# Performance work log

Measured on AMD Instinct MI355X. Metric: run time of the kernel, lower is better.

## Reference

```python
import jax, jax.numpy as jnp
import numpy as np

B, H, W, C = 16, 56, 56, 512
NUM_HEADS = 8
WS = 4  # window_size


def setup_inputs() -> dict:
    key = jax.random.key(0)
    k1, k2, k3, k4 = jax.random.split(key, 4)
    x = jax.random.normal(k1, (B, H, W, C), dtype=jnp.float32)
    w_qkv_h = jax.random.normal(k2, (3 * C, C), dtype=jnp.float32) * 0.02
    w_qkv_l = jax.random.normal(k3, (3 * C, C), dtype=jnp.float32) * 0.02
    w_proj = jax.random.normal(k4, (C, 2 * C), dtype=jnp.float32) * 0.02
    b_proj = jnp.zeros((C,), dtype=jnp.float32)
    return {"x": x, "w_qkv_h": w_qkv_h, "w_qkv_l": w_qkv_l,
            "w_proj": w_proj, "b_proj": b_proj}


def reference(x, w_qkv_h, w_qkv_l, w_proj, b_proj):
    b, h, w, c = x.shape
    nh = NUM_HEADS
    hd = c // nh
    nw = WS * WS  # tokens per window
    scale = c ** -0.5  # NOTE: original scales by full dim, not head dim

    # window partition: [B*H/ws*W/ws, ws*ws, C]
    xw = x.reshape(b, h // WS, WS, w // WS, WS, c)
    xw = xw.transpose(0, 1, 3, 2, 4, 5).reshape(-1, nw, c)

    # local branch qkv: [3, Nwin, nh, nw, hd]
    qkv_h = (xw @ w_qkv_h.T).reshape(-1, nw, 3, nh, hd).transpose(2, 0, 3, 1, 4)
    q_h, k_h, v_h = qkv_h[0], qkv_h[1], qkv_h[2]

    # global branch: average-pool each window to a single token [Nwin, 1, C]
    x_avg = x.reshape(b, h // WS, WS, w // WS, WS, c).mean(axis=(2, 4))
    x_avg = x_avg.reshape(-1, 1, c)
    qkv_l = (x_avg @ w_qkv_l.T).reshape(-1, 1, 3, nh, hd).transpose(2, 0, 3, 1, 4)
    q_l, k_l, v_l = qkv_l[0], qkv_l[1], qkv_l[2]

    # local window attention: [Nwin, nh, nw, nw]
    attn_h = jax.nn.softmax(jnp.einsum('bhqd,bhkd->bhqk', q_h, k_h) * scale, axis=-1)
    x_h = jnp.einsum('bhqk,bhkd->bhqd', attn_h, v_h)
    x_h = x_h.transpose(0, 2, 1, 3).reshape(-1, nw, c)

    # pooled global attention (1 token -> softmax over singleton = 1)
    attn_l = jax.nn.softmax(jnp.einsum('bhqd,bhkd->bhqk', q_l, k_l) * scale, axis=-1)
    x_l = jnp.einsum('bhqk,bhkd->bhqd', attn_l, v_l)
    x_l = x_l.transpose(0, 2, 1, 3).reshape(-1, 1, c)

    # concat local + broadcast global, project 2C -> C
    x_out = jnp.concatenate([x_h, jnp.broadcast_to(x_l, (x_l.shape[0], nw, c))], axis=-1)
    x_out = x_out @ w_proj.T + b_proj

    # window reverse
    x_out = x_out.reshape(b, h // WS, w // WS, WS, WS, c)
    x_out = x_out.transpose(0, 1, 3, 2, 4, 5).reshape(b, h, w, c)
    return x_out
```

## Files before the change

### kernel.cpp

```cpp
#include <hip/hip_runtime.h>


using bf16x8 = __attribute__((ext_vector_type(8))) short;
using f32x4  = __attribute__((ext_vector_type(4))) float;

#define SCALE 0.044194173824159216f

__device__ __forceinline__ unsigned short f2bf(float f) {
    union { float f; unsigned u; } v; v.f = f;
    unsigned u = v.u;
    return (unsigned short)((u + 0x7fffu + ((u >> 16) & 1u)) >> 16);
}

__device__ __forceinline__ void gl2lds16(const unsigned short* g, unsigned short* l) {
    __builtin_amdgcn_global_load_lds(
        (const __attribute__((address_space(1))) void*)g,
        (__attribute__((address_space(3))) void*)l, 16, 0, 0);
}

__global__ void k_prep_weights(const float* __restrict__ wqkv_h,
                               const float* __restrict__ wqkv_l,
                               const float* __restrict__ wproj,
                               unsigned short* __restrict__ WH,
                               unsigned short* __restrict__ WLV,
                               unsigned short* __restrict__ WP1,
                               unsigned short* __restrict__ WP2) {
    int i = blockIdx.x * 256 + threadIdx.x;
    if (i < 786432) {
        WH[i] = f2bf(wqkv_h[i]);
    } else {
        int j = i - 786432;
        int r = j >> 18;
        int t = j & 262143;
        int n = t >> 9, k = t & 511;
        if (r == 0)      WLV[t] = f2bf(wqkv_l[(1024 + n) * 512 + k]);
        else if (r == 1) WP1[t] = f2bf(wproj[n * 1024 + k]);
        else             WP2[t] = f2bf(wproj[n * 1024 + 512 + k]);
    }
}

__global__ void k_window_pool(const float* __restrict__ x,
                              unsigned short* __restrict__ XW,
                              unsigned short* __restrict__ XAVG) {
    int win = blockIdx.x * 2 + (threadIdx.x >> 7);
    int g = threadIdx.x & 127;
    int c = g * 4;
    int b = win / 196, rem = win % 196, wh = rem / 14, ww = rem % 14;
    float4 s = {0.f, 0.f, 0.f, 0.f};
    #pragma unroll
    for (int t = 0; t < 16; ++t) {
        int row = (b * 56 + wh * 4 + (t >> 2)) * 56 + ww * 4 + (t & 3);
        float4 v = *(const float4*)&x[(size_t)row * 512 + c];
        uint2 pk;
        pk.x = (unsigned)f2bf(v.x) | ((unsigned)f2bf(v.y) << 16);
        pk.y = (unsigned)f2bf(v.z) | ((unsigned)f2bf(v.w) << 16);
        *(uint2*)&XW[(size_t)(win * 16 + t) * 512 + c] = pk;
        s.x += v.x; s.y += v.y; s.z += v.z; s.w += v.w;
    }
    uint2 pa;
    pa.x = (unsigned)f2bf(s.x * 0.0625f) | ((unsigned)f2bf(s.y * 0.0625f) << 16);
    pa.y = (unsigned)f2bf(s.z * 0.0625f) | ((unsigned)f2bf(s.w * 0.0625f) << 16);
    *(uint2*)&XAVG[(size_t)win * 512 + c] = pa;
}

template <int NT>
__global__ void k_gemm512(const unsigned short* __restrict__ A,
                          const unsigned short* __restrict__ Bw,
                          unsigned short* __restrict__ outB,
                          float* __restrict__ outF,
                          const float* __restrict__ bias) {
    int wave = threadIdx.x >> 6, lane = threadIdx.x & 63;
    int quad = lane >> 4, l16 = lane & 15;
    int m0 = blockIdx.x * 64 + wave * 16;
    int n0 = blockIdx.y * (NT * 16);
    f32x4 acc[NT] = {};
    const unsigned short* arow = A + (size_t)(m0 + l16) * 512 + quad * 8;
    for (int kk = 0; kk < 16; ++kk) {
        bf16x8 a = *(const bf16x8*)(arow + kk * 32);
        #pragma unroll
        for (int nt = 0; nt < NT; ++nt) {
            bf16x8 b = *(const bf16x8*)(Bw + (size_t)(n0 + nt * 16 + l16) * 512 + kk * 32 + quad * 8);
            acc[nt] = __builtin_amdgcn_mfma_f32_16x16x32_bf16(a, b, acc[nt], 0, 0, 0);
        }
    }
    #pragma unroll
    for (int nt = 0; nt < NT; ++nt) {
        int col = n0 + nt * 16 + l16;
        float bv = (bias != nullptr) ? bias[col] : 0.f;
        #pragma unroll
        for (int r = 0; r < 4; ++r) {
            int row = m0 + quad * 4 + r;
            if (outF != nullptr) outF[(size_t)row * 512 + col] = acc[nt][r] + bv;
            else                 outB[(size_t)row * 512 + col] = f2bf(acc[nt][r]);
        }
    }
}

__global__ void __launch_bounds__(512, 4) k_fused(const unsigned short* __restrict__ XW,
                                                  const unsigned short* __restrict__ WH,
                                                  unsigned short* __restrict__ XH) {
    __shared__ __align__(16) char smem[81920];

    const int tid  = threadIdx.x;
    const int wave = tid >> 6, lane = tid & 63;
    const int quad = lane >> 4, l16 = lane & 15;
    const int mh = wave >> 2, nq = wave & 3;

    int id   = blockIdx.y * 392 + blockIdx.x;
    int s_   = id >> 3;
    int tb   = (id & 7) * 49 + (s_ >> 3);
    int head = s_ & 7;
    const int m0 = tb * 128;

    size_t aof[2];
    #pragma unroll
    for (int i = 0; i < 2; ++i) {
        int u = i * 512 + tid;
        int n = u >> 3;
        int gu = (u & 7) ^ (n & 7);
        aof[i] = (size_t)(m0 + n) * 512 + gu * 8;
    }
    size_t bof[3];
    #pragma unroll
    for (int i = 0; i < 3; ++i) {
        int u = i * 512 + tid;
        int n = u >> 3;
        int gu = (u & 7) ^ (n & 7);
        int nrow = (n >> 6) * 512 + head * 64 + (n & 63);
        bof[i] = (size_t)nrow * 512 + gu * 8;
    }

    unsigned short* const bufA[2] = { (unsigned short*)smem,
                                      (unsigned short*)(smem + 40960) };
    unsigned short* const bufB[2] = { (unsigned short*)(smem + 16384),
                                      (unsigned short*)(smem + 40960 + 16384) };

    f32x4 acc[4][3] = {};
    const int sx = l16 & 7;

    #pragma unroll
    for (int i = 0; i < 2; ++i)
        gl2lds16(XW + aof[i], bufA[0] + (i * 512 + wave * 64) * 8);
    #pragma unroll
    for (int i = 0; i < 3; ++i)
        gl2lds16(WH + bof[i], bufB[0] + (i * 512 + wave * 64) * 8);
    __syncthreads();

    #pragma unroll
    for (int ch = 0; ch < 8; ++ch) {
        unsigned short* As = bufA[ch & 1];
        unsigned short* Bs = bufB[ch & 1];
        if (ch < 7) {
            unsigned short* An = bufA[(ch + 1) & 1];
            unsigned short* Bn = bufB[(ch + 1) & 1];
            #pragma unroll
            for (int i = 0; i < 2; ++i)
                gl2lds16(XW + aof[i] + (ch + 1) * 64, An + (i * 512 + wave * 64) * 8);
            #pragma unroll
            for (int i = 0; i < 3; ++i)
                gl2lds16(WH + bof[i] + (ch + 1) * 64, Bn + (i * 512 + wave * 64) * 8);
        }
        #pragma unroll
        for (int kk = 0; kk < 2; ++kk) {
            int su = ((kk * 4 + quad) ^ sx) * 8;
            bf16x8 a[4], b[3];
            #pragma unroll
            for (int mf = 0; mf < 4; ++mf) {
                int row = mh * 64 + mf * 16 + l16;
                a[mf] = *(const bf16x8*)&As[row * 64 + (((kk * 4 + quad) ^ (row & 7)) ^ sx ^ (row & 7)) * 8];
            }
            #pragma unroll
            for (int j = 0; j < 3; ++j) {
                int brow = nq * 48 + j * 16 + l16;
                b[j] = *(const bf16x8*)&Bs[brow * 64 + (((kk * 4 + quad) ^ (brow & 7)) ^ sx ^ (brow & 7)) * 8];
            }
            #pragma unroll
            for (int mf = 0; mf < 4; ++mf)
                #pragma unroll
                for (int j = 0; j < 3; ++j)
                    acc[mf][j] = __builtin_amdgcn_mfma_f32_16x16x32_bf16(a[mf], b[j], acc[mf][j], 0, 0, 0);
        }
        __syncthreads();
    }

    {
        char* att = smem + mh * 33792;
        unsigned short* qs  = (unsigned short*)att;
        unsigned short* ks  = (unsigned short*)(att + 9216);
        unsigned short* vts = (unsigned short*)(att + 18432);
        #pragma unroll
        for (int j = 0; j < 3; ++j) {
            int cb = nq * 48 + j * 16;
            #pragma unroll
            for (int mf = 0; mf < 4; ++mf) {
                #pragma unroll
                for (int r = 0; r < 4; ++r) {
                    int tok = mf * 16 + quad * 4 + r;
                    unsigned short hv = f2bf(acc[mf][j][r]);
                    if (cb < 64)       qs[tok * 72 + cb + l16] = hv;
                    else if (cb < 128) ks[tok * 72 + (cb - 64) + l16] = hv;
                    else               vts[(cb - 128 + l16) * 88 + tok] = hv;
                }
            }
        }
    }
    __syncthreads();

    char* att = smem + (wave >> 2) * 33792;
    unsigned short* qs  = (unsigned short*)att;
    unsigned short* ks  = (unsigned short*)(att + 9216);
    unsigned short* vts = (unsigned short*)(att + 18432);
    unsigned short* Ps  = (unsigned short*)(att + 29696);
    const int lw = wave & 3, t0 = lw * 16;

    if (lw == 3) {
        #pragma unroll
        for (int i = 0; i < 16; ++i) vts[lane * 88 + 64 + i] = 0;
    }
    {
        int prow = lane >> 2, pc = 16 + (lane & 3) * 4;
        #pragma unroll
        for (int i = 0; i < 4; ++i) Ps[lw * 512 + prow * 32 + pc + i] = 0;
    }

    f32x4 sacc = {};
    {
        bf16x8 a0 = *(const bf16x8*)&qs[(t0 + l16) * 72 + quad * 8];
        bf16x8 b0 = *(const bf16x8*)&ks[(t0 + l16) * 72 + quad * 8];
        sacc = __builtin_amdgcn_mfma_f32_16x16x32_bf16(a0, b0, sacc, 0, 0, 0);
        bf16x8 a1 = *(const bf16x8*)&qs[(t0 + l16) * 72 + 32 + quad * 8];
        bf16x8 b1 = *(const bf16x8*)&ks[(t0 + l16) * 72 + 32 + quad * 8];
        sacc = __builtin_amdgcn_mfma_f32_16x16x32_bf16(a1, b1, sacc, 0, 0, 0);
    }
    float p[4];
    #pragma unroll
    for (int r = 0; r < 4; ++r) {
        float v = sacc[r] * SCALE;
        float m = v;
        m = fmaxf(m, __shfl_xor(m, 1));
        m = fmaxf(m, __shfl_xor(m, 2));
        m = fmaxf(m, __shfl_xor(m, 4));
        m = fmaxf(m, __shfl_xor(m, 8));
        float e = __expf(v - m);
        float sm = e;
        sm += __shfl_xor(sm, 1);
        sm += __shfl_xor(sm, 2);
        sm += __shfl_xor(sm, 4);
        sm += __shfl_xor(sm, 8);
        p[r] = e / sm;
    }
    #pragma unroll
    for (int r = 0; r < 4; ++r)
        Ps[lw * 512 + (quad * 4 + r) * 32 + l16] = f2bf(p[r]);

    bf16x8 pa = *(const bf16x8*)&Ps[lw * 512 + l16 * 32 + quad * 8];
    #pragma unroll
    for (int nt = 0; nt < 4; ++nt) {
        f32x4 y = {};
        bf16x8 bv = *(const bf16x8*)&vts[(nt * 16 + l16) * 88 + t0 + quad * 8];
        y = __builtin_amdgcn_mfma_f32_16x16x32_bf16(pa, bv, y, 0, 0, 0);
        #pragma unroll
        for (int r = 0; r < 4; ++r)
            XH[(size_t)(m0 + (wave >> 2) * 64 + t0 + quad * 4 + r) * 512 + head * 64 + nt * 16 + l16] = f2bf(y[r]);
    }
}

__global__ void __launch_bounds__(256, 2) k_gemm_proj(const unsigned short* __restrict__ XH,
                                                      const unsigned short* __restrict__ WP1,
                                                      const float* __restrict__ G,
                                                      float* __restrict__ out) {
    __shared__ __align__(16) char smem[65536];

    const int wave = threadIdx.x >> 6, lane = threadIdx.x & 63;
    const int quad = lane >> 4, l16 = lane & 15;

    int id = blockIdx.y * 392 + blockIdx.x;
    int s  = id >> 3;
    int xb = (id & 7) * 49 + (s >> 2);
    int yb = s & 3;
    const int m0 = xb * 128, n0 = yb * 128;
    const int wm = (wave >> 1) * 64;
    const int wn = (wave & 1) * 64;

    size_t aofs[4], bofs[4];
    #pragma unroll
    for (int i = 0; i < 4; ++i) {
        int u = (wave * 4 + i) * 64 + lane;
        int n = u >> 3;
        int gu = (lane & 7) ^ (n & 7);
        aofs[i] = (size_t)(m0 + n) * 512 + gu * 8;
        bofs[i] = (size_t)(n0 + n) * 512 + gu * 8;
    }

    unsigned short* const bufA[2] = { (unsigned short*)smem,
                                      (unsigned short*)(smem + 32768) };
    unsigned short* const bufB[2] = { (unsigned short*)(smem + 16384),
                                      (unsigned short*)(smem + 32768 + 16384) };

    f32x4 acc[4][4] = {};
    const int sx = l16 & 7;

    #pragma unroll
    for (int i = 0; i < 4; ++i) {
        gl2lds16(XH + aofs[i], bufA[0] + (wave * 4 + i) * 512);
        gl2lds16(WP1 + bofs[i], bufB[0] + (wave * 4 + i) * 512);
    }
    __syncthreads();

    #pragma unroll
    for (int ch = 0; ch < 8; ++ch) {
        unsigned short* As = bufA[ch & 1];
        unsigned short* Bs = bufB[ch & 1];
        if (ch < 7) {
            unsigned short* An = bufA[(ch + 1) & 1];
            unsigned short* Bn = bufB[(ch + 1) & 1];
            #pragma unroll
            for (int i = 0; i < 4; ++i) {
                gl2lds16(XH + aofs[i] + (ch + 1) * 64, An + (wave * 4 + i) * 512);
                gl2lds16(WP1 + bofs[i] + (ch + 1) * 64, Bn + (wave * 4 + i) * 512);
            }
        }
        #pragma unroll
        for (int kk = 0; kk < 2; ++kk) {
            int su = ((kk * 4 + quad) ^ sx) * 8;
            bf16x8 a[4], b[4];
            #pragma unroll
            for (int mf = 0; mf < 4; ++mf)
                a[mf] = *(const bf16x8*)&As[(wm + mf * 16 + l16) * 64 + su];
            #pragma unroll
            for (int j = 0; j < 4; ++j)
                b[j] = *(const bf16x8*)&Bs[(wn + j * 16 + l16) * 64 + su];
            #pragma unroll
            for (int mf = 0; mf < 4; ++mf)
                #pragma unroll
                for (int j = 0; j < 4; ++j)
                    acc[mf][j] = __builtin_amdgcn_mfma_f32_16x16x32_bf16(a[mf], b[j], acc[mf][j], 0, 0, 0);
        }
        __syncthreads();
    }

    #pragma unroll
    for (int mf = 0; mf < 4; ++mf) {
        #pragma unroll
        for (int r = 0; r < 4; ++r) {
            int tl  = wm + mf * 16 + quad * 4 + r;
            int gt  = m0 + tl;
            int win = gt >> 4, tw = gt & 15;
            int bb = win / 196, rem = win % 196;
            int wh = rem / 14, ww = rem % 14;
            int orow = (bb * 56 + wh * 4 + (tw >> 2)) * 56 + ww * 4 + (tw & 3);
            #pragma unroll
            for (int j = 0; j < 4; ++j) {
                int ncol = n0 + wn + j * 16 + l16;
                out[(size_t)orow * 512 + ncol] = acc[mf][j][r] + G[(size_t)win * 512 + ncol];
            }
        }
    }
}

extern "C" void kernel_launch(void* const* d_in, const int* in_sizes, int n_in,
                              void* d_out, int out_size, void* d_ws, size_t ws_size,
                              hipStream_t stream) {
    const float* x      = (const float*)d_in[0];
    const float* wqkv_h = (const float*)d_in[1];
    const float* wqkv_l = (const float*)d_in[2];
    const float* wproj  = (const float*)d_in[3];
    const float* bproj  = (const float*)d_in[4];
    float* out = (float*)d_out;

    char* ws = (char*)d_ws;
    unsigned short* WH   = (unsigned short*)(ws + 0);
    unsigned short* WLV  = (unsigned short*)(ws + 1572864);
    unsigned short* WP1  = (unsigned short*)(ws + 2097152);
    unsigned short* WP2  = (unsigned short*)(ws + 2621440);
    unsigned short* XW   = (unsigned short*)(ws + 3145728);
    unsigned short* XAVG = (unsigned short*)(ws + 54525952);
    unsigned short* VL   = (unsigned short*)(ws + 57737216);
    float*          G    = (float*)(ws + 60948480);
    unsigned short* XH   = (unsigned short*)(ws + 67371008);

    k_prep_weights<<<dim3(6144), dim3(256), 0, stream>>>(wqkv_h, wqkv_l, wproj, WH, WLV, WP1, WP2);
    k_window_pool<<<dim3(1568), dim3(256), 0, stream>>>(x, XW, XAVG);
    k_gemm512<2><<<dim3(49, 16), dim3(256), 0, stream>>>(XAVG, WLV, VL, (float*)nullptr, (const float*)nullptr);
    k_gemm512<2><<<dim3(49, 16), dim3(256), 0, stream>>>(VL, WP2, (unsigned short*)nullptr, G, bproj);
    k_fused<<<dim3(392, 8), dim3(512), 0, stream>>>(XW, WH, XH);
    k_gemm_proj<<<dim3(392, 4), dim3(256), 0, stream>>>(XH, WP1, G, out);
}
```

Baseline: 392.5 us.

## Double fused QKV tile to 256 tokens per block and relax pipeline waits

The fused QKV+attention kernel now processes 256 tokens per block instead of 128, with each wave covering 96 QKV columns. This halves the grid and reuses each weight tile across twice as many rows, at the cost of more LDS (128KB) and accumulator registers, so fewer blocks fit per CU. Both the fused and projection GEMM loops replace __syncthreads with explicit vmcnt/lgkmcnt waits plus raw barriers, so the prefetch of the next chunk can stay in flight. Offsets switch from size_t to int to save address arithmetic.

```diff
diff --git a/kernel.cpp b/kernel.cpp
--- a/kernel.cpp
+++ b/kernel.cpp
@@ -96,101 +96,95 @@
     }
 }
 
-__global__ void __launch_bounds__(512, 4) k_fused(const unsigned short* __restrict__ XW,
+__global__ void __launch_bounds__(512, 2) k_fused(const unsigned short* __restrict__ XW,
                                                   const unsigned short* __restrict__ WH,
                                                   unsigned short* __restrict__ XH) {
-    __shared__ __align__(16) char smem[81920];
+    __shared__ __align__(16) char smem[131072];
 
     const int tid  = threadIdx.x;
     const int wave = tid >> 6, lane = tid & 63;
     const int quad = lane >> 4, l16 = lane & 15;
-    const int mh = wave >> 2, nq = wave & 3;
-
-    int id   = blockIdx.y * 392 + blockIdx.x;
-    int s_   = id >> 3;
-    int tb   = (id & 7) * 49 + (s_ >> 3);
-    int head = s_ & 7;
-    const int m0 = tb * 128;
-
-    size_t aof[2];
-    #pragma unroll
-    for (int i = 0; i < 2; ++i) {
+    const int mh = wave >> 1, nq = wave & 1;
+
+    int id   = blockIdx.y * 196 + blockIdx.x;
+    int w_   = (id & 7) * 196 + (id >> 3);
+    int tb   = w_ >> 3, head = w_ & 7;
+    const int m0 = tb * 256;
+
+    int aof[4];
+    #pragma unroll
+    for (int i = 0; i < 4; ++i) {
         int u = i * 512 + tid;
         int n = u >> 3;
         int gu = (u & 7) ^ (n & 7);
-        aof[i] = (size_t)(m0 + n) * 512 + gu * 8;
-    }
-    size_t bof[3];
+        aof[i] = (m0 + n) * 512 + gu * 8;
+    }
+    int bof[3];
     #pragma unroll
     for (int i = 0; i < 3; ++i) {
         int u = i * 512 + tid;
         int n = u >> 3;
         int gu = (u & 7) ^ (n & 7);
         int nrow = (n >> 6) * 512 + head * 64 + (n & 63);
-        bof[i] = (size_t)nrow * 512 + gu * 8;
-    }
-
-    unsigned short* const bufA[2] = { (unsigned short*)smem,
-                                      (unsigned short*)(smem + 40960) };
-    unsigned short* const bufB[2] = { (unsigned short*)(smem + 16384),
-                                      (unsigned short*)(smem + 40960 + 16384) };
-
-    f32x4 acc[4][3] = {};
+        bof[i] = nrow * 512 + gu * 8;
+    }
+
+    f32x4 acc[4][6] = {};
     const int sx = l16 & 7;
 
-    #pragma unroll
-    for (int i = 0; i < 2; ++i)
-        gl2lds16(XW + aof[i], bufA[0] + (i * 512 + wave * 64) * 8);
-    #pragma unroll
-    for (int i = 0; i < 3; ++i)
-        gl2lds16(WH + bof[i], bufB[0] + (i * 512 + wave * 64) * 8);
-    __syncthreads();
+    {
+        unsigned short* A0 = (unsigned short*)smem;
+        unsigned short* B0 = (unsigned short*)(smem + 32768);
+        #pragma unroll
+        for (int i = 0; i < 4; ++i) gl2lds16(XW + aof[i], A0 + (i * 512 + wave * 64) * 8);
+        #pragma unroll
+        for (int i = 0; i < 3; ++i) gl2lds16(WH + bof[i], B0 + (i * 512 + wave * 64) * 8);
+    }
 
     #pragma unroll
     for (int ch = 0; ch < 8; ++ch) {
-        unsigned short* As = bufA[ch & 1];
-        unsigned short* Bs = bufB[ch & 1];
         if (ch < 7) {
-            unsigned short* An = bufA[(ch + 1) & 1];
-            unsigned short* Bn = bufB[(ch + 1) & 1];
-            #pragma unroll
-            for (int i = 0; i < 2; ++i)
-                gl2lds16(XW + aof[i] + (ch + 1) * 64, An + (i * 512 + wave * 64) * 8);
-            #pragma unroll
-            for (int i = 0; i < 3; ++i)
-                gl2lds16(WH + bof[i] + (ch + 1) * 64, Bn + (i * 512 + wave * 64) * 8);
-        }
+            unsigned short* An = (unsigned short*)(smem + ((ch + 1) & 1) * 57344);
+            unsigned short* Bn = (unsigned short*)(smem + ((ch + 1) & 1) * 57344 + 32768);
+            #pragma unroll
+            for (int i = 0; i < 4; ++i) gl2lds16(XW + aof[i] + (ch + 1) * 64, An + (i * 512 + wave * 64) * 8);
+            #pragma unroll
+            for (int i = 0; i < 3; ++i) gl2lds16(WH + bof[i] + (ch + 1) * 64, Bn + (i * 512 + wave * 64) * 8);
+        }
+        if (ch < 7) asm volatile("s_waitcnt vmcnt(7)" ::: "memory");
+        else        asm volatile("s_waitcnt vmcnt(0)" ::: "memory");
+        __builtin_amdgcn_s_barrier();
+
+        unsigned short* As = (unsigned short*)(smem + (ch & 1) * 57344);
+        unsigned short* Bs = (unsigned short*)(smem + (ch & 1) * 57344 + 32768);
         #pragma unroll
         for (int kk = 0; kk < 2; ++kk) {
             int su = ((kk * 4 + quad) ^ sx) * 8;
-            bf16x8 a[4], b[3];
-            #pragma unroll
-            for (int mf = 0; mf < 4; ++mf) {
-                int row = mh * 64 + mf * 16 + l16;
-                a[mf] = *(const bf16x8*)&As[row * 64 + (((kk * 4 + quad) ^ (row & 7)) ^ sx ^ (row & 7)) * 8];
-            }
-            #pragma unroll
-            for (int j = 0; j < 3; ++j) {
-                int brow = nq * 48 + j * 16 + l16;
-                b[j] = *(const bf16x8*)&Bs[brow * 64 + (((kk * 4 + quad) ^ (brow & 7)) ^ sx ^ (brow & 7)) * 8];
-            }
+            bf16x8 a[4], b[6];
+            #pragma unroll
+            for (int mf = 0; mf < 4; ++mf)
+                a[mf] = *(const bf16x8*)&As[(mh * 64 + mf * 16 + l16) * 64 + su];
+            #pragma unroll
+            for (int j = 0; j < 6; ++j)
+                b[j] = *(const bf16x8*)&Bs[(nq * 96 + j * 16 + l16) * 64 + su];
             #pragma unroll
             for (int mf = 0; mf < 4; ++mf)
                 #pragma unroll
-                for (int j = 0; j < 3; ++j)
+                for (int j = 0; j < 6; ++j)
                     acc[mf][j] = __builtin_amdgcn_mfma_f32_16x16x32_bf16(a[mf], b[j], acc[mf][j], 0, 0, 0);
         }
-        __syncthreads();
+        asm volatile("s_waitcnt lgkmcnt(0)" ::: "memory");
+        __builtin_amdgcn_s_barrier();
     }
 
     {
-        char* att = smem + mh * 33792;
+        char* att = smem + mh * 32768;
         unsigned short* qs  = (unsigned short*)att;
         unsigned short* ks  = (unsigned short*)(att + 9216);
         unsigned short* vts = (unsigned short*)(att + 18432);
         #pragma unroll
-        for (int j = 0; j < 3; ++j) {
-            int cb = nq * 48 + j * 16;
+        for (int j = 0; j < 6; ++j) {
+            int cb = nq * 96 + j * 16;
             #pragma unroll
             for (int mf = 0; mf < 4; ++mf) {
                 #pragma unroll
@@ -199,69 +193,75 @@
                     unsigned short hv = f2bf(acc[mf][j][r]);
                     if (cb < 64)       qs[tok * 72 + cb + l16] = hv;
                     else if (cb < 128) ks[tok * 72 + (cb - 64) + l16] = hv;
-                    else               vts[(cb - 128 + l16) * 88 + tok] = hv;
+                    else               vts[(cb - 128 + l16) * 80 + tok] = hv;
                 }
             }
         }
     }
     __syncthreads();
 
-    char* att = smem + (wave >> 2) * 33792;
+    char* att = smem + (wave >> 1) * 32768;
     unsigned short* qs  = (unsigned short*)att;
     unsigned short* ks  = (unsigned short*)(att + 9216);
     unsigned short* vts = (unsigned short*)(att + 18432);
-    unsigned short* Ps  = (unsigned short*)(att + 29696);
-    const int lw = wave & 3, t0 = lw * 16;
-
-    if (lw == 3) {
-        #pragma unroll
-        for (int i = 0; i < 16; ++i) vts[lane * 88 + 64 + i] = 0;
-    }
-    {
-        int prow = lane >> 2, pc = 16 + (lane & 3) * 4;
-        #pragma unroll
-        for (int i = 0; i < 4; ++i) Ps[lw * 512 + prow * 32 + pc + i] = 0;
-    }
-
-    f32x4 sacc = {};
-    {
-        bf16x8 a0 = *(const bf16x8*)&qs[(t0 + l16) * 72 + quad * 8];
-        bf16x8 b0 = *(const bf16x8*)&ks[(t0 + l16) * 72 + quad * 8];
-        sacc = __builtin_amdgcn_mfma_f32_16x16x32_bf16(a0, b0, sacc, 0, 0, 0);
-        bf16x8 a1 = *(const bf16x8*)&qs[(t0 + l16) * 72 + 32 + quad * 8];
-        bf16x8 b1 = *(const bf16x8*)&ks[(t0 + l16) * 72 + 32 + quad * 8];
-        sacc = __builtin_amdgcn_mfma_f32_16x16x32_bf16(a1, b1, sacc, 0, 0, 0);
-    }
-    float p[4];
-    #pragma unroll
-    for (int r = 0; r < 4; ++r) {
-        float v = sacc[r] * SCALE;
-        float m = v;
-        m = fmaxf(m, __shfl_xor(m, 1));
-        m = fmaxf(m, __shfl_xor(m, 2));
-        m = fmaxf(m, __shfl_xor(m, 4));
-        m = fmaxf(m, __shfl_xor(m, 8));
-        float e = __expf(v - m);
-        float sm = e;
-        sm += __shfl_xor(sm, 1);
-        sm += __shfl_xor(sm, 2);
-        sm += __shfl_xor(sm, 4);
-        sm += __shfl_xor(sm, 8);
-        p[r] = e / sm;
-    }
-    #pragma unroll
-    for (int r = 0; r < 4; ++r)
-        Ps[lw * 512 + (quad * 4 + r) * 32 + l16] = f2bf(p[r]);
-
-    bf16x8 pa = *(const bf16x8*)&Ps[lw * 512 + l16 * 32 + quad * 8];
-    #pragma unroll
-    for (int nt = 0; nt < 4; ++nt) {
-        f32x4 y = {};
-        bf16x8 bv = *(const bf16x8*)&vts[(nt * 16 + l16) * 88 + t0 + quad * 8];
-        y = __builtin_amdgcn_mfma_f32_16x16x32_bf16(pa, bv, y, 0, 0, 0);
+    unsigned short* Ps  = (unsigned short*)(att + 28672);
+    const int set = wave >> 1;
+
+    #pragma unroll
+    for (int sub = 0; sub < 2; ++sub) {
+        const int lw = (wave & 1) * 2 + sub;
+        const int t0 = lw * 16;
+
+        if (lw == 3) {
+            #pragma unroll
+            for (int i = 0; i < 16; ++i) vts[lane * 80 + 64 + i] = 0;
+        }
+        {
+            int prow = lane >> 2, pc = 16 + (lane & 3) * 4;
+            #pragma unroll
+            for (int i = 0; i < 4; ++i) Ps[lw * 512 + prow * 32 + pc + i] = 0;
+        }
+
+        f32x4 sacc = {};
+        {
+            bf16x8 a0 = *(const bf16x8*)&qs[(t0 + l16) * 72 + quad * 8];
+            bf16x8 b0 = *(const bf16x8*)&ks[(t0 + l16) * 72 + quad * 8];
+            sacc = __builtin_amdgcn_mfma_f32_16x16x32_bf16(a0, b0, sacc, 0, 0, 0);
+            bf16x8 a1 = *(const bf16x8*)&qs[(t0 + l16) * 72 + 32 + quad * 8];
+            bf16x8 b1 = *(const bf16x8*)&ks[(t0 + l16) * 72 + 32 + quad * 8];
+            sacc = __builtin_amdgcn_mfma_f32_16x16x32_bf16(a1, b1, sacc, 0, 0, 0);
+        }
+        float p[4];
+        #pragma unroll
+        for (int r = 0; r < 4; ++r) {
+            float v = sacc[r] * SCALE;
+            float m = v;
+            m = fmaxf(m, __shfl_xor(m, 1));
+            m = fmaxf(m, __shfl_xor(m, 2));
+            m = fmaxf(m, __shfl_xor(m, 4));
+            m = fmaxf(m, __shfl_xor(m, 8));
+            float e = __expf(v - m);
+            float sm = e;
+            sm += __shfl_xor(sm, 1);
+            sm += __shfl_xor(sm, 2);
+            sm += __shfl_xor(sm, 4);
+            sm += __shfl_xor(sm, 8);
+            p[r] = e / sm;
+        }
         #pragma unroll
         for (int r = 0; r < 4; ++r)
-            XH[(size_t)(m0 + (wave >> 2) * 64 + t0 + quad * 4 + r) * 512 + head * 64 + nt * 16 + l16] = f2bf(y[r]);
+            Ps[lw * 512 + (quad * 4 + r) * 32 + l16] = f2bf(p[r]);
+
+        bf16x8 pa = *(const bf16x8*)&Ps[lw * 512 + l16 * 32 + quad * 8];
+        #pragma unroll
+        for (int nt = 0; nt < 4; ++nt) {
+            f32x4 y = {};
+            bf16x8 bv = *(const bf16x8*)&vts[(nt * 16 + l16) * 80 + t0 + quad * 8];
+            y = __builtin_amdgcn_mfma_f32_16x16x32_bf16(pa, bv, y, 0, 0, 0);
+            #pragma unroll
+            for (int r = 0; r < 4; ++r)
+                XH[(size_t)(m0 + set * 64 + t0 + quad * 4 + r) * 512 + head * 64 + nt * 16 + l16] = f2bf(y[r]);
+        }
     }
 }
 
@@ -282,14 +282,14 @@
     const int wm = (wave >> 1) * 64;
     const int wn = (wave & 1) * 64;
 
-    size_t aofs[4], bofs[4];
+    int aofs[4], bofs[4];
     #pragma unroll
     for (int i = 0; i < 4; ++i) {
         int u = (wave * 4 + i) * 64 + lane;
         int n = u >> 3;
         int gu = (lane & 7) ^ (n & 7);
-        aofs[i] = (size_t)(m0 + n) * 512 + gu * 8;
-        bofs[i] = (size_t)(n0 + n) * 512 + gu * 8;
+        aofs[i] = (m0 + n) * 512 + gu * 8;
+        bofs[i] = (n0 + n) * 512 + gu * 8;
     }
 
     unsigned short* const bufA[2] = { (unsigned short*)smem,
@@ -305,12 +305,9 @@
         gl2lds16(XH + aofs[i], bufA[0] + (wave * 4 + i) * 512);
         gl2lds16(WP1 + bofs[i], bufB[0] + (wave * 4 + i) * 512);
     }
-    __syncthreads();
 
     #pragma unroll
     for (int ch = 0; ch < 8; ++ch) {
-        unsigned short* As = bufA[ch & 1];
-        unsigned short* Bs = bufB[ch & 1];
         if (ch < 7) {
             unsigned short* An = bufA[(ch + 1) & 1];
             unsigned short* Bn = bufB[(ch + 1) & 1];
@@ -320,6 +317,12 @@
                 gl2lds16(WP1 + bofs[i] + (ch + 1) * 64, Bn + (wave * 4 + i) * 512);
             }
         }
+        if (ch < 7) asm volatile("s_waitcnt vmcnt(8)" ::: "memory");
+        else        asm volatile("s_waitcnt vmcnt(0)" ::: "memory");
+        __builtin_amdgcn_s_barrier();
+
+        unsigned short* As = bufA[ch & 1];
+        unsigned short* Bs = bufB[ch & 1];
         #pragma unroll
         for (int kk = 0; kk < 2; ++kk) {
             int su = ((kk * 4 + quad) ^ sx) * 8;
@@ -336,7 +339,8 @@
                 for (int j = 0; j < 4; ++j)
                     acc[mf][j] = __builtin_amdgcn_mfma_f32_16x16x32_bf16(a[mf], b[j], acc[mf][j], 0, 0, 0);
         }
-        __syncthreads();
+        asm volatile("s_waitcnt lgkmcnt(0)" ::: "memory");
+        __builtin_amdgcn_s_barrier();
     }
 
     #pragma unroll
@@ -383,6 +387,6 @@
     k_window_pool<<<dim3(1568), dim3(256), 0, stream>>>(x, XW, XAVG);
     k_gemm512<2><<<dim3(49, 16), dim3(256), 0, stream>>>(XAVG, WLV, VL, (float*)nullptr, (const float*)nullptr);
     k_gemm512<2><<<dim3(49, 16), dim3(256), 0, stream>>>(VL, WP2, (unsigned short*)nullptr, G, bproj);
-    k_fused<<<dim3(392, 8), dim3(512), 0, stream>>>(XW, WH, XH);
+    k_fused<<<dim3(196, 8), dim3(512), 0, stream>>>(XW, WH, XH);
     k_gemm_proj<<<dim3(392, 4), dim3(256), 0, stream>>>(XH, WP1, G, out);
 }
```

After: 390.3 us. Within noise of the previous version (-0.6%).
